# Kernel optimization log

Measured on AMD Instinct MI355X. Metric: run time of the kernel, lower is better.

The kernel has to match this reference:

```python
import jax, jax.numpy as jnp
import numpy as np
import math

B, S, E, H, DFF = 4, 1024, 1024, 16, 4096
HD = E // H
EPS = 1e-8


def setup_inputs() -> dict:
    key = jax.random.key(0)
    ks = jax.random.split(key, 16)
    sc = 0.02
    inp = {
        'x': jax.random.normal(ks[0], (B, S, E), jnp.float32),
        'mask': jax.random.randint(ks[1], (B, S, S), 0, 2, jnp.int32),
        'Wq': jax.random.normal(ks[2], (E, E), jnp.float32) * sc,
        'bq': jnp.zeros((E,), jnp.float32),
        'Wk': jax.random.normal(ks[3], (E, E), jnp.float32) * sc,
        'bk': jnp.zeros((E,), jnp.float32),
        'Wv': jax.random.normal(ks[4], (E, E), jnp.float32) * sc,
        'bv': jnp.zeros((E,), jnp.float32),
        'Wo': jax.random.normal(ks[5], (E, E), jnp.float32) * sc,
        'bo': jnp.zeros((E,), jnp.float32),
        'W1': jax.random.normal(ks[6], (DFF, E), jnp.float32) * sc,
        'b1': jnp.zeros((DFF,), jnp.float32),
        'W2': jax.random.normal(ks[7], (E, DFF), jnp.float32) * sc,
        'b2': jnp.zeros((E,), jnp.float32),
        'g1': jnp.ones((E,), jnp.float32),
        'be1': jnp.zeros((E,), jnp.float32),
        'g2': jnp.ones((E,), jnp.float32),
        'be2': jnp.zeros((E,), jnp.float32),
    }
    return inp


def _layernorm(x, g, b):
    # torch LayerNorm here: (x-mean)/(std+eps), std is unbiased (ddof=1)
    mean = jnp.mean(x, axis=-1, keepdims=True)
    std = jnp.std(x, axis=-1, keepdims=True, ddof=1)
    return g * (x - mean) / (std + EPS) + b


def _gelu(x):
    c = math.sqrt(2.0 / math.pi)
    return 0.5 * x * (1.0 + jnp.tanh(c * (x + 0.044715 * x ** 3)))


def _block(x, mask_f, Wq, bq, Wk, bk, Wv, bv, Wo, bo, W1, b1, W2, b2, g1, be1, g2, be2):
    # --- attention sublayer (pre-norm, residual) ---
    nx = _layernorm(x, g1, be1)
    q = (nx @ Wq.T + bq).reshape(B, S, H, HD).transpose(0, 2, 1, 3)  # [B,H,S,D]
    k = (nx @ Wk.T + bk).reshape(B, S, H, HD).transpose(0, 2, 1, 3)
    v = (nx @ Wv.T + bv).reshape(B, S, H, HD).transpose(0, 2, 1, 3)
    scores = jnp.einsum('bhqd,bhkd->bhqk', q, k) / math.sqrt(HD)
    m = mask_f[:, None, :, :]  # [B,1,S,S]
    scores = jnp.where(m == 0, jnp.float32(-0.01), scores * m)
    p = jax.nn.softmax(scores, axis=-1)
    o = jnp.einsum('bhqk,bhkd->bhqd', p, v)  # [B,H,S,D]
    o = o.transpose(0, 2, 1, 3).reshape(B, S, E)
    x = x + (o @ Wo.T + bo)
    # --- FFN sublayer ---
    nx2 = _layernorm(x, g2, be2)
    ff = _gelu(nx2 @ W1.T + b1) @ W2.T + b2
    return x + ff


def reference(x, mask, Wq, bq, Wk, bk, Wv, bv, Wo, bo, W1, b1, W2, b2, g1, be1, g2, be2):
    mask_f = mask.astype(jnp.float32)
    return _block(x, mask_f, Wq, bq, Wk, bk, Wv, bv, Wo, bo, W1, b1, W2, b2, g1, be1, g2, be2)
```

## Files before the change

kernel.cpp:

```cpp
#include <hip/hip_runtime.h>
#include <math.h>

typedef __attribute__((ext_vector_type(8))) short short8;
typedef __attribute__((ext_vector_type(4))) float f32x4;
typedef __attribute__((ext_vector_type(4))) int   i32x4v;

#define B_   4
#define S_   1024
#define E_   1024
#define H_   16
#define DFF_ 4096

#define HB_MAX 4.0f

__device__ __forceinline__ ushort f2bf(float f){
  unsigned int x = __float_as_uint(f);
  x += 0x7fffu + ((x >> 16) & 1u);
  return (ushort)(x >> 16);
}

__device__ __forceinline__ float gelu_f(float x){
  const float c = 0.7978845608028654f;
  float u = 2.0f * c * (x + 0.044715f * x * x * x);
  return x / (1.0f + __expf(-u));
}

__device__ __forceinline__ void gl2lds16(const void* g, void* l){
  __builtin_amdgcn_global_load_lds(
      (const __attribute__((address_space(1))) void*)g,
      (__attribute__((address_space(3))) void*)l, 16, 0, 0);
}

__device__ __forceinline__ int q8(float x, float s){
  float v = fmaxf(fminf(x * s, 127.f), -127.f);
  return ((int)__builtin_rintf(v)) & 255;
}
__device__ __forceinline__ int pk_i8x4(float a, float b, float c, float d, float s){
  return q8(a,s) | (q8(b,s) << 8) | (q8(c,s) << 16) | (q8(d,s) << 24);
}

__global__ __launch_bounds__(256) void prep_kernel(
    const float* __restrict__ Wq, const float* __restrict__ Wk,
    const float* __restrict__ Wv, const float* __restrict__ Wo,
    const float* __restrict__ W1, const float* __restrict__ W2,
    const float* __restrict__ bq, const float* __restrict__ bk,
    const float* __restrict__ bv, const int* __restrict__ mask,
    unsigned char* __restrict__ bQKV8, float* __restrict__ sQKV,
    ushort* __restrict__ bWo,
    unsigned char* __restrict__ bW18, float* __restrict__ sW1,
    unsigned char* __restrict__ bW28, float* __restrict__ sW2,
    float* __restrict__ cbias, unsigned long long* __restrict__ maskp)
{
  int blk = blockIdx.x, t = threadIdx.x;
  __shared__ float sm[4];

  if (blk < 4096){
    float4 v = ((const float4*)(W1 + (size_t)blk * 1024))[t];
    float m = fmaxf(fmaxf(fabsf(v.x), fabsf(v.y)), fmaxf(fabsf(v.z), fabsf(v.w)));
    #pragma unroll
    for (int o = 32; o; o >>= 1) m = fmaxf(m, __shfl_xor(m, o));
    if ((t & 63) == 0) sm[t >> 6] = m;
    __syncthreads();
    float mx = fmaxf(fmaxf(sm[0], sm[1]), fmaxf(sm[2], sm[3])) + 1e-20f;
    float qs = 127.0f / mx;
    ((int*)(bW18 + (size_t)blk * 1024))[t] = pk_i8x4(v.x, v.y, v.z, v.w, qs);
    if (t == 0) sW1[blk] = mx * (1.0f / 127.0f);
    return;
  }
  if (blk < 5120){
    int r = blk - 4096;
    float4 v[4]; float m = 0.f;
    #pragma unroll
    for (int i = 0; i < 4; i++){
      v[i] = ((const float4*)(W2 + (size_t)r * 4096))[t + i * 256];
      m = fmaxf(m, fmaxf(fmaxf(fabsf(v[i].x), fabsf(v[i].y)), fmaxf(fabsf(v[i].z), fabsf(v[i].w))));
    }
    #pragma unroll
    for (int o = 32; o; o >>= 1) m = fmaxf(m, __shfl_xor(m, o));
    if ((t & 63) == 0) sm[t >> 6] = m;
    __syncthreads();
    float mx = fmaxf(fmaxf(sm[0], sm[1]), fmaxf(sm[2], sm[3])) + 1e-20f;
    float qs = 127.0f / mx;
    #pragma unroll
    for (int i = 0; i < 4; i++)
      ((int*)(bW28 + (size_t)r * 4096))[t + i * 256] = pk_i8x4(v[i].x, v[i].y, v[i].z, v[i].w, qs);
    if (t == 0) sW2[r] = mx * (1.0f / 127.0f);
    return;
  }
  if (blk < 8192){
    int r = blk - 5120;
    const float* src = (r < 1024) ? Wq + (size_t)r * 1024
                     : (r < 2048) ? Wk + (size_t)(r - 1024) * 1024
                                  : Wv + (size_t)(r - 2048) * 1024;
    float4 v = ((const float4*)src)[t];
    float m = fmaxf(fmaxf(fabsf(v.x), fabsf(v.y)), fmaxf(fabsf(v.z), fabsf(v.w)));
    #pragma unroll
    for (int o = 32; o; o >>= 1) m = fmaxf(m, __shfl_xor(m, o));
    if ((t & 63) == 0) sm[t >> 6] = m;
    __syncthreads();
    float mx = fmaxf(fmaxf(sm[0], sm[1]), fmaxf(sm[2], sm[3])) + 1e-20f;
    float qs = 127.0f / mx;
    ((int*)(bQKV8 + (size_t)r * 1024))[t] = pk_i8x4(v.x, v.y, v.z, v.w, qs);
    if (t == 0) sQKV[r] = mx * (1.0f / 127.0f);
    return;
  }
  if (blk < 9216){
    int j = (blk - 8192) * 256 + t;
    float4 v = ((const float4*)Wo)[j];
    ushort4 o; o.x = f2bf(v.x); o.y = f2bf(v.y); o.z = f2bf(v.z); o.w = f2bf(v.w);
    ((ushort4*)bWo)[j] = o;
    return;
  }
  if (blk == 9216){
    #pragma unroll
    for (int r = 0; r < 12; r++){
      int idx = r * 256 + t;
      cbias[idx] = (idx < 1024) ? bq[idx] : (idx < 2048 ? bk[idx - 1024] : bv[idx - 2048]);
    }
    return;
  }
  int widx = (blk - 9217) * 4 + (t >> 6);
  int mv = mask[(size_t)widx * 64 + (t & 63)];
  unsigned long long bal = __ballot(mv != 0);
  if ((t & 63) == 0) maskp[widx] = bal;
}

__global__ __launch_bounds__(256) void ln_i8(const float* __restrict__ x,
    const float* __restrict__ g, const float* __restrict__ be,
    unsigned char* __restrict__ out8, float* __restrict__ sOut){
  int row = blockIdx.x, t = threadIdx.x;
  float4 v = ((const float4*)(x + (size_t)row * E_))[t];
  float s = v.x + v.y + v.z + v.w;
  float q = v.x*v.x + v.y*v.y + v.z*v.z + v.w*v.w;
  #pragma unroll
  for (int o = 32; o; o >>= 1){ s += __shfl_xor(s, o); q += __shfl_xor(q, o); }
  __shared__ float ss[4], sq[4], sm[4];
  int w = t >> 6;
  if ((t & 63) == 0){ ss[w] = s; sq[w] = q; }
  __syncthreads();
  s = ss[0] + ss[1] + ss[2] + ss[3];
  q = sq[0] + sq[1] + sq[2] + sq[3];
  float mean = s * (1.0f / E_);
  float var  = fmaxf((q - (float)E_ * mean * mean) * (1.0f / (E_ - 1)), 0.0f);
  float inv = 1.0f / (sqrtf(var) + 1e-8f);
  float4 gv = ((const float4*)g)[t];
  float4 bv = ((const float4*)be)[t];
  float n0 = gv.x * (v.x - mean) * inv + bv.x;
  float n1 = gv.y * (v.y - mean) * inv + bv.y;
  float n2 = gv.z * (v.z - mean) * inv + bv.z;
  float n3 = gv.w * (v.w - mean) * inv + bv.w;
  float m = fmaxf(fmaxf(fabsf(n0), fabsf(n1)), fmaxf(fabsf(n2), fabsf(n3)));
  #pragma unroll
  for (int o = 32; o; o >>= 1) m = fmaxf(m, __shfl_xor(m, o));
  if ((t & 63) == 0) sm[w] = m;
  __syncthreads();
  float mx = fmaxf(fmaxf(sm[0], sm[1]), fmaxf(sm[2], sm[3])) + 1e-20f;
  float qs = 127.0f / mx;
  ((int*)(out8 + (size_t)row * E_))[t] = pk_i8x4(n0, n1, n2, n3, qs);
  if (t == 0) sOut[row] = mx * (1.0f / 127.0f);
}

__global__ __launch_bounds__(256) void ln2_fuse(const float* __restrict__ x,
    const float* __restrict__ P, const float* __restrict__ bo,
    const float* __restrict__ g, const float* __restrict__ be,
    float* __restrict__ x2, unsigned char* __restrict__ nx28, float* __restrict__ sOut){
  int row = blockIdx.x, t = threadIdx.x;
  size_t idx = (size_t)row * 256 + t;
  float4 v  = ((const float4*)x)[idx];
  float4 p0 = ((const float4*)P)[idx];
  float4 p1 = ((const float4*)P)[idx + 1048576];
  float4 bv0 = ((const float4*)bo)[t];
  v.x += p0.x + p1.x + bv0.x;
  v.y += p0.y + p1.y + bv0.y;
  v.z += p0.z + p1.z + bv0.z;
  v.w += p0.w + p1.w + bv0.w;
  ((float4*)x2)[idx] = v;
  float s = v.x + v.y + v.z + v.w;
  float q = v.x*v.x + v.y*v.y + v.z*v.z + v.w*v.w;
  #pragma unroll
  for (int o = 32; o; o >>= 1){ s += __shfl_xor(s, o); q += __shfl_xor(q, o); }
  __shared__ float ss[4], sq[4], sm[4];
  int w = t >> 6;
  if ((t & 63) == 0){ ss[w] = s; sq[w] = q; }
  __syncthreads();
  s = ss[0] + ss[1] + ss[2] + ss[3];
  q = sq[0] + sq[1] + sq[2] + sq[3];
  float mean = s * (1.0f / E_);
  float var  = fmaxf((q - (float)E_ * mean * mean) * (1.0f / (E_ - 1)), 0.0f);
  float inv = 1.0f / (sqrtf(var) + 1e-8f);
  float4 gv = ((const float4*)g)[t];
  float4 bev = ((const float4*)be)[t];
  float n0 = gv.x * (v.x - mean) * inv + bev.x;
  float n1 = gv.y * (v.y - mean) * inv + bev.y;
  float n2 = gv.z * (v.z - mean) * inv + bev.z;
  float n3 = gv.w * (v.w - mean) * inv + bev.w;
  float m = fmaxf(fmaxf(fabsf(n0), fabsf(n1)), fmaxf(fabsf(n2), fabsf(n3)));
  #pragma unroll
  for (int o = 32; o; o >>= 1) m = fmaxf(m, __shfl_xor(m, o));
  if ((t & 63) == 0) sm[w] = m;
  __syncthreads();
  float mx = fmaxf(fmaxf(sm[0], sm[1]), fmaxf(sm[2], sm[3])) + 1e-20f;
  float qs = 127.0f / mx;
  ((int*)(nx28 + (size_t)row * E_))[t] = pk_i8x4(n0, n1, n2, n3, qs);
  if (t == 0) sOut[row] = mx * (1.0f / 127.0f);
}

__global__ __launch_bounds__(256) void reduce_out(const float* __restrict__ x2,
    const float* __restrict__ P, const float* __restrict__ b2, float* __restrict__ out){
  size_t i = (size_t)blockIdx.x * 256 + threadIdx.x;
  int col4 = i & 255;
  float4 v  = ((const float4*)x2)[i];
  float4 p0 = ((const float4*)P)[i];
  float4 p1 = ((const float4*)P)[i + 1048576];
  float4 bv = ((const float4*)b2)[col4];
  float4 o;
  o.x = v.x + p0.x + p1.x + bv.x;
  o.y = v.y + p0.y + p1.y + bv.y;
  o.z = v.z + p0.z + p1.z + bv.z;
  o.w = v.w + p0.w + p1.w + bv.w;
  ((float4*)out)[i] = o;
}

template<int MODE>
__global__ __launch_bounds__(256) void gemm_i8(
    const unsigned char* __restrict__ A8, const unsigned char* __restrict__ B8,
    const float* __restrict__ sA, const float* __restrict__ sB,
    const float* __restrict__ bias,
    ushort* __restrict__ Cb, unsigned char* __restrict__ C8, float* __restrict__ Pf,
    int K, int ldc)
{
  __shared__ __align__(16) unsigned char As[128 * 128];
  __shared__ __align__(16) unsigned char Bs[128 * 128];
  const int t = threadIdx.x, w = t >> 6, ln = t & 63;
  const int quad = ln >> 4, lc = ln & 15;
  const int wm = w >> 1, wn = w & 1;
  const int m0 = blockIdx.y * 128, n0 = blockIdx.x * 128;
  int kbeg = 0, kend = K;
  if (MODE == 2){
    int kh = K >> 1;
    kbeg = blockIdx.z * kh; kend = kbeg + kh;
    Pf += (size_t)blockIdx.z * (4096 * 1024);
  }

  i32x4v acc[4][4];
  #pragma unroll
  for (int i = 0; i < 4; i++)
    #pragma unroll
    for (int j = 0; j < 4; j++) acc[i][j] = i32x4v{0, 0, 0, 0};

  for (int k0 = kbeg; k0 < kend; k0 += 128){
    __syncthreads();
    #pragma unroll
    for (int r2 = 0; r2 < 4; r2++){
      int chunk = r2 * 256 + t;
      int row = chunk >> 3, co = (chunk & 7) * 16;
      gl2lds16(A8 + (size_t)(m0 + row) * K + k0 + co, As + (size_t)(r2*256 + (t & 192)) * 16);
      gl2lds16(B8 + (size_t)(n0 + row) * K + k0 + co, Bs + (size_t)(r2*256 + (t & 192)) * 16);
    }
    __syncthreads();
    #pragma unroll
    for (int kk = 0; kk < 128; kk += 64){
      i32x4v af[4], bfr[4];
      #pragma unroll
      for (int i = 0; i < 4; i++)
        af[i]  = *(const i32x4v*)(As + (size_t)(wm*64 + i*16 + lc) * 128 + kk + quad*16);
      #pragma unroll
      for (int j = 0; j < 4; j++)
        bfr[j] = *(const i32x4v*)(Bs + (size_t)(wn*64 + j*16 + lc) * 128 + kk + quad*16);
      #pragma unroll
      for (int i = 0; i < 4; i++)
        #pragma unroll
        for (int j = 0; j < 4; j++)
          acc[i][j] = __builtin_amdgcn_mfma_i32_16x16x64_i8(af[i], bfr[j], acc[i][j], 0, 0, 0);
    }
  }

  #pragma unroll
  for (int j = 0; j < 4; j++){
    int col = n0 + wn*64 + j*16 + lc;
    float sb = sB[col];
    float bc = (MODE == 2) ? 0.f : bias[col];
    #pragma unroll
    for (int i = 0; i < 4; i++){
      int row0 = m0 + wm*64 + i*16 + quad*4;
      #pragma unroll
      for (int r = 0; r < 4; r++){
        int row = row0 + r;
        if (MODE == 0){
          float v = (float)acc[i][j][r] * sA[row] * sb + bc;
          float sc = (col < 1024) ? 0.125f : 1.0f;
          Cb[(size_t)row * ldc + col] = f2bf(v * sc);
        } else if (MODE == 1){
          float v = gelu_f((float)acc[i][j][r] * sA[row] * sb + bc);
          C8[(size_t)row * 4096 + col] = (unsigned char)q8(v, 127.0f / HB_MAX);
        } else {
          Pf[(size_t)row * 1024 + col] = (float)acc[i][j][r] * (HB_MAX / 127.0f) * sb;
        }
      }
    }
  }
}

__global__ __launch_bounds__(256) void gemm_sk(
    const ushort* __restrict__ A, const ushort* __restrict__ Bm,
    float* __restrict__ P, int K)
{
  __shared__ __align__(16) ushort As[128 * 64];
  __shared__ __align__(16) ushort Bs[128 * 64];
  const int t = threadIdx.x, w = t >> 6, ln = t & 63;
  const int quad = ln >> 4, lc = ln & 15;
  const int wm = w >> 1, wn = w & 1;
  const int m0 = blockIdx.y * 128, n0 = blockIdx.x * 128;
  const int kh = K >> 1;
  const int kbase = blockIdx.z * kh;
  float* Pz = P + (size_t)blockIdx.z * (4096 * 1024);

  f32x4 acc[4][4];
  #pragma unroll
  for (int i = 0; i < 4; i++)
    #pragma unroll
    for (int j = 0; j < 4; j++) acc[i][j] = f32x4{0.f, 0.f, 0.f, 0.f};

  for (int k0 = kbase; k0 < kbase + kh; k0 += 64){
    __syncthreads();
    #pragma unroll
    for (int r2 = 0; r2 < 4; r2++){
      int chunk = r2 * 256 + t;
      int row = chunk >> 3, co = (chunk & 7) * 8;
      gl2lds16(A  + (size_t)(m0 + row) * K + k0 + co, As + (size_t)(r2*256 + (t & 192)) * 8);
    }
    #pragma unroll
    for (int r2 = 0; r2 < 4; r2++){
      int chunk = r2 * 256 + t;
      int row = chunk >> 3, co = (chunk & 7) * 8;
      gl2lds16(Bm + (size_t)(n0 + row) * K + k0 + co, Bs + (size_t)(r2*256 + (t & 192)) * 8);
    }
    __syncthreads();
    #pragma unroll
    for (int kk = 0; kk < 64; kk += 32){
      short8 af[4], bfr[4];
      #pragma unroll
      for (int i = 0; i < 4; i++)
        af[i]  = *(const short8*)(As + (wm*64 + i*16 + lc) * 64 + kk + quad*8);
      #pragma unroll
      for (int j = 0; j < 4; j++)
        bfr[j] = *(const short8*)(Bs + (wn*64 + j*16 + lc) * 64 + kk + quad*8);
      #pragma unroll
      for (int i = 0; i < 4; i++)
        #pragma unroll
        for (int j = 0; j < 4; j++)
          acc[i][j] = __builtin_amdgcn_mfma_f32_16x16x32_bf16(af[i], bfr[j], acc[i][j], 0, 0, 0);
    }
  }

  #pragma unroll
  for (int j = 0; j < 4; j++){
    int col = n0 + wn*64 + j*16 + lc;
    #pragma unroll
    for (int i = 0; i < 4; i++){
      int row0 = m0 + wm*64 + i*16 + quad*4;
      #pragma unroll
      for (int r = 0; r < 4; r++)
        Pz[(size_t)(row0 + r) * 1024 + col] = acc[i][j][r];
    }
  }
}

__global__ __launch_bounds__(256) void vT_kernel(const ushort* __restrict__ QKV,
                                                 ushort* __restrict__ Vt){
  __shared__ ushort tile[64][68];
  int st = blockIdx.x;
  int bh = blockIdx.y;
  int b = bh >> 4, h = bh & 15;
  int t = threadIdx.x;
  #pragma unroll
  for (int it = 0; it < 4; it++){
    int idx = it * 256 + t;
    int r = idx >> 4, c4 = (idx & 15) * 4;
    ushort4 v = *(const ushort4*)(QKV + ((size_t)(b*1024 + st*64 + r)) * 3072 + 2048 + h*64 + c4);
    *(ushort4*)(&tile[r][c4]) = v;
  }
  __syncthreads();
  #pragma unroll
  for (int it = 0; it < 4; it++){
    int idx = it * 256 + t;
    int d = idx >> 4, s4 = (idx & 15) * 4;
    ushort4 o;
    o.x = tile[s4+0][d]; o.y = tile[s4+1][d]; o.z = tile[s4+2][d]; o.w = tile[s4+3][d];
    *(ushort4*)(Vt + ((size_t)bh * 64 + d) * 1024 + st*64 + s4) = o;
  }
}

__global__ __launch_bounds__(256) void attn_kernel(
    const ushort* __restrict__ QKV, const ushort* __restrict__ Vt,
    const unsigned long long* __restrict__ maskp, ushort* __restrict__ O)
{
  __shared__ __align__(16) ushort Ks[64 * 64];
  __shared__ __align__(16) ushort Vs[64 * 64];
  __shared__ __align__(16) ushort Ps[4][16 * 72];

  const int t = threadIdx.x, w = t >> 6, ln = t & 63;
  const int quad = ln >> 4, lc = ln & 15;
  const int bh = blockIdx.x, b = bh >> 4;
  const int q0 = blockIdx.y * 64;
  const int coff = (bh & 15) * 64;
  const size_t rb = (size_t)b * S_;

  const int myq = q0 + w*16 + lc;
  const ushort* qrow = QKV + (rb + myq) * 3072 + coff;
  short8 qf0 = *(const short8*)(qrow + quad*8);
  short8 qf1 = *(const short8*)(qrow + 32 + quad*8);
  const unsigned long long* mrow = maskp + (rb + myq) * 16;

  f32x4 of[4];
  #pragma unroll
  for (int gd = 0; gd < 4; gd++) of[gd] = f32x4{0.f, 0.f, 0.f, 0.f};
  float lsum = 0.0f;
  const float PM = 0.99004983f;

  for (int k0 = 0; k0 < S_; k0 += 64){
    __syncthreads();
    #pragma unroll
    for (int it = 0; it < 2; it++){
      int chunk = it * 256 + t;
      int row = chunk >> 3, blk = chunk & 7;
      int dst = row * 64 + ((blk ^ (row & 7)) * 8);
      *(short8*)(Ks + dst) = *(const short8*)(QKV + (rb + k0 + row) * 3072 + 1024 + coff + blk*8);
      *(short8*)(Vs + dst) = *(const short8*)(Vt + ((size_t)bh * 64 + row) * 1024 + k0 + blk*8);
    }
    unsigned long long m64 = mrow[k0 >> 6];
    __syncthreads();

    f32x4 sf[4];
    #pragma unroll
    for (int g = 0; g < 4; g++){
      int krow = g*16 + lc;
      short8 kf0 = *(const short8*)(Ks + krow*64 + ((quad       ^ (lc & 7)) * 8));
      short8 kf1 = *(const short8*)(Ks + krow*64 + (((4 + quad) ^ (lc & 7)) * 8));
      f32x4 z = f32x4{0.f, 0.f, 0.f, 0.f};
      z = __builtin_amdgcn_mfma_f32_16x16x32_bf16(kf0, qf0, z, 0, 0, 0);
      z = __builtin_amdgcn_mfma_f32_16x16x32_bf16(kf1, qf1, z, 0, 0, 0);
      sf[g] = z;
    }

    #pragma unroll
    for (int g = 0; g < 4; g++){
      unsigned int b4 = (unsigned int)(m64 >> (g*16 + quad*4)) & 0xFu;
      float p0 = (b4 & 1u) ? __expf(sf[g][0]) : PM;
      float p1 = (b4 & 2u) ? __expf(sf[g][1]) : PM;
      float p2 = (b4 & 4u) ? __expf(sf[g][2]) : PM;
      float p3 = (b4 & 8u) ? __expf(sf[g][3]) : PM;
      lsum += p0 + p1 + p2 + p3;
      ushort4 pw; pw.x = f2bf(p0); pw.y = f2bf(p1); pw.z = f2bf(p2); pw.w = f2bf(p3);
      *(ushort4*)(&Ps[w][lc*72 + g*16 + quad*4]) = pw;
    }

    short8 pf0 = *(const short8*)(&Ps[w][lc*72 + quad*8]);
    short8 pf1 = *(const short8*)(&Ps[w][lc*72 + 32 + quad*8]);
    #pragma unroll
    for (int gd = 0; gd < 4; gd++){
      int vrow = gd*16 + lc;
      short8 vf0 = *(const short8*)(Vs + vrow*64 + ((quad       ^ (lc & 7)) * 8));
      short8 vf1 = *(const short8*)(Vs + vrow*64 + (((4 + quad) ^ (lc & 7)) * 8));
      of[gd] = __builtin_amdgcn_mfma_f32_16x16x32_bf16(vf0, pf0, of[gd], 0, 0, 0);
      of[gd] = __builtin_amdgcn_mfma_f32_16x16x32_bf16(vf1, pf1, of[gd], 0, 0, 0);
    }
  }

  lsum += __shfl_xor(lsum, 16);
  lsum += __shfl_xor(lsum, 32);
  float inv = 1.0f / lsum;

  ushort* orow = O + (rb + myq) * E_ + coff;
  #pragma unroll
  for (int gd = 0; gd < 4; gd++){
    ushort4 o4;
    o4.x = f2bf(of[gd][0] * inv);
    o4.y = f2bf(of[gd][1] * inv);
    o4.z = f2bf(of[gd][2] * inv);
    o4.w = f2bf(of[gd][3] * inv);
    *(ushort4*)(orow + gd*16 + quad*4) = o4;
  }
}

extern "C" void kernel_launch(void* const* d_in, const int* in_sizes, int n_in,
                              void* d_out, int out_size, void* d_ws, size_t ws_size,
                              hipStream_t stream)
{
  const float* x   = (const float*)d_in[0];
  const int*   mask= (const int*)  d_in[1];
  const float* Wq  = (const float*)d_in[2];
  const float* bq  = (const float*)d_in[3];
  const float* Wk  = (const float*)d_in[4];
  const float* bk  = (const float*)d_in[5];
  const float* Wv  = (const float*)d_in[6];
  const float* bv  = (const float*)d_in[7];
  const float* Wo  = (const float*)d_in[8];
  const float* bo  = (const float*)d_in[9];
  const float* W1  = (const float*)d_in[10];
  const float* b1  = (const float*)d_in[11];
  const float* W2  = (const float*)d_in[12];
  const float* b2  = (const float*)d_in[13];
  const float* g1  = (const float*)d_in[14];
  const float* be1 = (const float*)d_in[15];
  const float* g2  = (const float*)d_in[16];
  const float* be2 = (const float*)d_in[17];
  float* out = (float*)d_out;

  char* ws = (char*)d_ws;
  size_t off = 0;
  auto alloc = [&](size_t bytes) -> void* {
    void* p = ws + off; off += (bytes + 255) & ~(size_t)255; return p;
  };
  const size_t MM = 1024 * 1024;
  unsigned char* bQKV8 = (unsigned char*)alloc(3 * MM);
  float* sQKV  = (float*)alloc(3072 * 4);
  ushort* bWo  = (ushort*)alloc(MM * 2);
  unsigned char* bW18 = (unsigned char*)alloc(4 * MM);
  float* sW1   = (float*)alloc(4096 * 4);
  unsigned char* bW28 = (unsigned char*)alloc(4 * MM);
  float* sW2   = (float*)alloc(1024 * 4);
  float* cbias = (float*)alloc(3072 * 4);
  unsigned long long* maskp = (unsigned long long*)alloc(65536 * 8);
  unsigned char* nx8  = (unsigned char*)alloc(4 * MM);
  float* sX1   = (float*)alloc(4096 * 4);
  ushort* QKV  = (ushort*)alloc(12 * MM * 2);
  ushort* VtG  = (ushort*)alloc(4 * MM * 2);
  ushort* Ob   = (ushort*)alloc(4 * MM * 2);
  float*  x2   = (float*) alloc(4 * MM * 4);
  unsigned char* nx28 = (unsigned char*)alloc(4 * MM);
  float* sX2   = (float*)alloc(4096 * 4);
  unsigned char* hb8  = (unsigned char*)alloc(16 * MM);

  float* Pbuf = (float*)nx8;

  prep_kernel<<<25601, 256, 0, stream>>>(Wq, Wk, Wv, Wo, W1, W2, bq, bk, bv, mask,
                                         bQKV8, sQKV, bWo, bW18, sW1, bW28, sW2,
                                         cbias, maskp);

  ln_i8<<<4096, 256, 0, stream>>>(x, g1, be1, nx8, sX1);

  gemm_i8<0><<<dim3(24, 32), 256, 0, stream>>>(
      nx8, bQKV8, sX1, sQKV, cbias, QKV, nullptr, nullptr, 1024, 3072);

  vT_kernel<<<dim3(16, 64), 256, 0, stream>>>(QKV, VtG);

  attn_kernel<<<dim3(64, 16), 256, 0, stream>>>(QKV, VtG, maskp, Ob);

  gemm_sk<<<dim3(8, 32, 2), 256, 0, stream>>>(Ob, bWo, Pbuf, 1024);

  ln2_fuse<<<4096, 256, 0, stream>>>(x, Pbuf, bo, g2, be2, x2, nx28, sX2);

  gemm_i8<1><<<dim3(32, 32), 256, 0, stream>>>(
      nx28, bW18, sX2, sW1, b1, nullptr, hb8, nullptr, 1024, 4096);

  gemm_i8<2><<<dim3(8, 32, 2), 256, 0, stream>>>(
      hb8, bW28, nullptr, sW2, nullptr, nullptr, nullptr, Pbuf, 4096, 1024);

  reduce_out<<<4096, 256, 0, stream>>>(x2, Pbuf, b2, out);
}
```

Baseline: 333.6 us.

## Quantize attention output and Wo to int8 and reuse int8 GEMM for projection

Wo is now quantized per row to int8 with scales in the prep kernel. The attention kernel writes its output as int8, using the fixed HB_MAX scale, instead of bf16. The output projection then runs through the existing split-K int8 GEMM (mode 2) in place of the bf16 MFMA GEMM, which is removed. The attention P tile is also packed to bf16 by truncation with a perm instruction rather than round-to-nearest. This halves the attention output traffic and uses faster int8 MFMA, but a fixed clamp scale of 4 on attention outputs risks accuracy loss.

New measurement: 325.8 us. 2.3% less time.

```diff
diff --git a/kernel.cpp b/kernel.cpp
--- a/kernel.cpp
+++ b/kernel.cpp
@@ -17,6 +17,10 @@
   unsigned int x = __float_as_uint(f);
   x += 0x7fffu + ((x >> 16) & 1u);
   return (ushort)(x >> 16);
+}
+
+__device__ __forceinline__ unsigned int pk_bf16_trunc(float a, float b){
+  return __builtin_amdgcn_perm(__float_as_uint(b), __float_as_uint(a), 0x07060302u);
 }
 
 __device__ __forceinline__ float gelu_f(float x){
@@ -46,7 +50,7 @@
     const float* __restrict__ bq, const float* __restrict__ bk,
     const float* __restrict__ bv, const int* __restrict__ mask,
     unsigned char* __restrict__ bQKV8, float* __restrict__ sQKV,
-    ushort* __restrict__ bWo,
+    unsigned char* __restrict__ bWo8, float* __restrict__ sWo,
     unsigned char* __restrict__ bW18, float* __restrict__ sW1,
     unsigned char* __restrict__ bW28, float* __restrict__ sW2,
     float* __restrict__ cbias, unsigned long long* __restrict__ maskp)
@@ -105,10 +109,17 @@
     return;
   }
   if (blk < 9216){
-    int j = (blk - 8192) * 256 + t;
-    float4 v = ((const float4*)Wo)[j];
-    ushort4 o; o.x = f2bf(v.x); o.y = f2bf(v.y); o.z = f2bf(v.z); o.w = f2bf(v.w);
-    ((ushort4*)bWo)[j] = o;
+    int r = blk - 8192;
+    float4 v = ((const float4*)(Wo + (size_t)r * 1024))[t];
+    float m = fmaxf(fmaxf(fabsf(v.x), fabsf(v.y)), fmaxf(fabsf(v.z), fabsf(v.w)));
+    #pragma unroll
+    for (int o = 32; o; o >>= 1) m = fmaxf(m, __shfl_xor(m, o));
+    if ((t & 63) == 0) sm[t >> 6] = m;
+    __syncthreads();
+    float mx = fmaxf(fmaxf(sm[0], sm[1]), fmaxf(sm[2], sm[3])) + 1e-20f;
+    float qs = 127.0f / mx;
+    ((int*)(bWo8 + (size_t)r * 1024))[t] = pk_i8x4(v.x, v.y, v.z, v.w, qs);
+    if (t == 0) sWo[r] = mx * (1.0f / 127.0f);
     return;
   }
   if (blk == 9216){
@@ -301,71 +312,6 @@
   }
 }
 
-__global__ __launch_bounds__(256) void gemm_sk(
-    const ushort* __restrict__ A, const ushort* __restrict__ Bm,
-    float* __restrict__ P, int K)
-{
-  __shared__ __align__(16) ushort As[128 * 64];
-  __shared__ __align__(16) ushort Bs[128 * 64];
-  const int t = threadIdx.x, w = t >> 6, ln = t & 63;
-  const int quad = ln >> 4, lc = ln & 15;
-  const int wm = w >> 1, wn = w & 1;
-  const int m0 = blockIdx.y * 128, n0 = blockIdx.x * 128;
-  const int kh = K >> 1;
-  const int kbase = blockIdx.z * kh;
-  float* Pz = P + (size_t)blockIdx.z * (4096 * 1024);
-
-  f32x4 acc[4][4];
-  #pragma unroll
-  for (int i = 0; i < 4; i++)
-    #pragma unroll
-    for (int j = 0; j < 4; j++) acc[i][j] = f32x4{0.f, 0.f, 0.f, 0.f};
-
-  for (int k0 = kbase; k0 < kbase + kh; k0 += 64){
-    __syncthreads();
-    #pragma unroll
-    for (int r2 = 0; r2 < 4; r2++){
-      int chunk = r2 * 256 + t;
-      int row = chunk >> 3, co = (chunk & 7) * 8;
-      gl2lds16(A  + (size_t)(m0 + row) * K + k0 + co, As + (size_t)(r2*256 + (t & 192)) * 8);
-    }
-    #pragma unroll
-    for (int r2 = 0; r2 < 4; r2++){
-      int chunk = r2 * 256 + t;
-      int row = chunk >> 3, co = (chunk & 7) * 8;
-      gl2lds16(Bm + (size_t)(n0 + row) * K + k0 + co, Bs + (size_t)(r2*256 + (t & 192)) * 8);
-    }
-    __syncthreads();
-    #pragma unroll
-    for (int kk = 0; kk < 64; kk += 32){
-      short8 af[4], bfr[4];
-      #pragma unroll
-      for (int i = 0; i < 4; i++)
-        af[i]  = *(const short8*)(As + (wm*64 + i*16 + lc) * 64 + kk + quad*8);
-      #pragma unroll
-      for (int j = 0; j < 4; j++)
-        bfr[j] = *(const short8*)(Bs + (wn*64 + j*16 + lc) * 64 + kk + quad*8);
-      #pragma unroll
-      for (int i = 0; i < 4; i++)
-        #pragma unroll
-        for (int j = 0; j < 4; j++)
-          acc[i][j] = __builtin_amdgcn_mfma_f32_16x16x32_bf16(af[i], bfr[j], acc[i][j], 0, 0, 0);
-    }
-  }
-
-  #pragma unroll
-  for (int j = 0; j < 4; j++){
-    int col = n0 + wn*64 + j*16 + lc;
-    #pragma unroll
-    for (int i = 0; i < 4; i++){
-      int row0 = m0 + wm*64 + i*16 + quad*4;
-      #pragma unroll
-      for (int r = 0; r < 4; r++)
-        Pz[(size_t)(row0 + r) * 1024 + col] = acc[i][j][r];
-    }
-  }
-}
-
 __global__ __launch_bounds__(256) void vT_kernel(const ushort* __restrict__ QKV,
                                                  ushort* __restrict__ Vt){
   __shared__ ushort tile[64][68];
@@ -393,7 +339,7 @@
 
 __global__ __launch_bounds__(256) void attn_kernel(
     const ushort* __restrict__ QKV, const ushort* __restrict__ Vt,
-    const unsigned long long* __restrict__ maskp, ushort* __restrict__ O)
+    const unsigned long long* __restrict__ maskp, unsigned char* __restrict__ O8)
 {
   __shared__ __align__(16) ushort Ks[64 * 64];
   __shared__ __align__(16) ushort Vs[64 * 64];
@@ -451,8 +397,10 @@
       float p2 = (b4 & 4u) ? __expf(sf[g][2]) : PM;
       float p3 = (b4 & 8u) ? __expf(sf[g][3]) : PM;
       lsum += p0 + p1 + p2 + p3;
-      ushort4 pw; pw.x = f2bf(p0); pw.y = f2bf(p1); pw.z = f2bf(p2); pw.w = f2bf(p3);
-      *(ushort4*)(&Ps[w][lc*72 + g*16 + quad*4]) = pw;
+      uint2 pw;
+      pw.x = pk_bf16_trunc(p0, p1);
+      pw.y = pk_bf16_trunc(p2, p3);
+      *(uint2*)(&Ps[w][lc*72 + g*16 + quad*4]) = pw;
     }
 
     short8 pf0 = *(const short8*)(&Ps[w][lc*72 + quad*8]);
@@ -471,15 +419,12 @@
   lsum += __shfl_xor(lsum, 32);
   float inv = 1.0f / lsum;
 
-  ushort* orow = O + (rb + myq) * E_ + coff;
+  unsigned char* orow = O8 + (rb + myq) * E_ + coff;
   #pragma unroll
   for (int gd = 0; gd < 4; gd++){
-    ushort4 o4;
-    o4.x = f2bf(of[gd][0] * inv);
-    o4.y = f2bf(of[gd][1] * inv);
-    o4.z = f2bf(of[gd][2] * inv);
-    o4.w = f2bf(of[gd][3] * inv);
-    *(ushort4*)(orow + gd*16 + quad*4) = o4;
+    int pk = pk_i8x4(of[gd][0] * inv, of[gd][1] * inv,
+                     of[gd][2] * inv, of[gd][3] * inv, 127.0f / HB_MAX);
+    *(int*)(orow + gd*16 + quad*4) = pk;
   }
 }
 
@@ -515,7 +460,8 @@
   const size_t MM = 1024 * 1024;
   unsigned char* bQKV8 = (unsigned char*)alloc(3 * MM);
   float* sQKV  = (float*)alloc(3072 * 4);
-  ushort* bWo  = (ushort*)alloc(MM * 2);
+  unsigned char* bWo8 = (unsigned char*)alloc(MM);
+  float* sWo   = (float*)alloc(1024 * 4);
   unsigned char* bW18 = (unsigned char*)alloc(4 * MM);
   float* sW1   = (float*)alloc(4096 * 4);
   unsigned char* bW28 = (unsigned char*)alloc(4 * MM);
@@ -526,7 +472,7 @@
   float* sX1   = (float*)alloc(4096 * 4);
   ushort* QKV  = (ushort*)alloc(12 * MM * 2);
   ushort* VtG  = (ushort*)alloc(4 * MM * 2);
-  ushort* Ob   = (ushort*)alloc(4 * MM * 2);
+  unsigned char* Ob8 = (unsigned char*)alloc(4 * MM);
   float*  x2   = (float*) alloc(4 * MM * 4);
   unsigned char* nx28 = (unsigned char*)alloc(4 * MM);
   float* sX2   = (float*)alloc(4096 * 4);
@@ -535,7 +481,7 @@
   float* Pbuf = (float*)nx8;
 
   prep_kernel<<<25601, 256, 0, stream>>>(Wq, Wk, Wv, Wo, W1, W2, bq, bk, bv, mask,
-                                         bQKV8, sQKV, bWo, bW18, sW1, bW28, sW2,
+                                         bQKV8, sQKV, bWo8, sWo, bW18, sW1, bW28, sW2,
                                          cbias, maskp);
 
   ln_i8<<<4096, 256, 0, stream>>>(x, g1, be1, nx8, sX1);
@@ -545,9 +491,10 @@
 
   vT_kernel<<<dim3(16, 64), 256, 0, stream>>>(QKV, VtG);
 
-  attn_kernel<<<dim3(64, 16), 256, 0, stream>>>(QKV, VtG, maskp, Ob);
-
-  gemm_sk<<<dim3(8, 32, 2), 256, 0, stream>>>(Ob, bWo, Pbuf, 1024);
+  attn_kernel<<<dim3(64, 16), 256, 0, stream>>>(QKV, VtG, maskp, Ob8);
+
+  gemm_i8<2><<<dim3(8, 32, 2), 256, 0, stream>>>(
+      Ob8, bWo8, nullptr, sWo, nullptr, nullptr, nullptr, Pbuf, 1024, 1024);
 
   ln2_fuse<<<4096, 256, 0, stream>>>(x, Pbuf, bo, g2, be2, x2, nx28, sX2);
 
```
